# Performance work log

Measured on AMD Instinct MI355X. Metric: run time of the kernel, lower is better.

The kernel has to match this reference:

```python
import jax, jax.numpy as jnp
import numpy as np

B, K, D = 16384, 32, 64
N_USERS, N_ENT, N_REL = 100000, 100000, 32
MAX_NORM = 1.0


def renorm(e):
    # emulate torch nn.Embedding(max_norm=1): rescale rows with norm > 1
    n = jnp.linalg.norm(e, axis=-1, keepdims=True)
    return e * jnp.minimum(1.0, MAX_NORM / jnp.maximum(n, 1e-7))


def setup_inputs() -> dict:
    key = jax.random.key(0)
    ks = jax.random.split(key, 9)
    return {
        "user_table": jax.random.normal(ks[0], (N_USERS, D), dtype=jnp.float32),
        "entity_table": jax.random.normal(ks[1], (N_ENT, D), dtype=jnp.float32),
        "relation_table": jax.random.normal(ks[2], (N_REL, D), dtype=jnp.float32),
        "W": jax.random.normal(ks[3], (D, D), dtype=jnp.float32) / np.sqrt(D),
        "b": jnp.zeros((D,), dtype=jnp.float32),
        "users": jax.random.randint(ks[4], (B,), 0, N_USERS),
        "items": jax.random.randint(ks[5], (B,), 0, N_ENT),
        "adj_entity": jax.random.randint(ks[6], (N_ENT, K), 0, N_ENT),
        "adj_relation": jax.random.randint(ks[7], (N_ENT, K), 0, N_REL),
    }


def reference(user_table, entity_table, relation_table, W, b,
              users, items, adj_entity, adj_relation):
    # neighbor id gather: [B, K]
    nbr_ent_ids = adj_entity[items]
    nbr_rel_ids = adj_relation[items]
    # embedding lookups with max_norm renorm
    user_emb = renorm(user_table[users])                 # [B, D]
    item_emb = renorm(entity_table[items])               # [B, D]
    nbr_ent = renorm(entity_table[nbr_ent_ids])          # [B, K, D]
    nbr_rel = renorm(relation_table[nbr_rel_ids])        # [B, K, D]
    # user-relation attention scores, softmax over neighbors
    scores = jnp.einsum('bd,bkd->bk', user_emb, nbr_rel)  # [B, K]
    attn = jax.nn.softmax(scores, axis=-1)
    # attention-weighted neighbor aggregation
    nbr_vec = jnp.einsum('bk,bkd->bd', attn, nbr_ent)     # [B, D]
    # sum aggregator + linear + relu (dropout omitted: eval-mode baseline)
    out = item_emb + nbr_vec
    out = jax.nn.relu(out @ W.T + b)
    return (user_emb, out)
```

## Files before the change

kernel.cpp:

```cpp
#include <hip/hip_runtime.h>
#include <math.h>

#define BB 16384
#define KK_N 32
#define DD 64
#define N_ENT 100000
#define N_REL 32

#define WS_REL_OFF_BYTES ((size_t)N_ENT * DD * 2)
#define WS_NEED_BYTES (WS_REL_OFF_BYTES + (size_t)N_REL * DD * 4)

#define PT_ENT  N_ENT
#define PT_USER (N_ENT + BB)
#define PT_ALL  (N_ENT + BB + N_REL)

typedef _Float16 f16x8 __attribute__((ext_vector_type(8)));
typedef _Float16 f16x4 __attribute__((ext_vector_type(4)));
typedef float    f32x4 __attribute__((ext_vector_type(4)));

__device__ __forceinline__ float dot4(float4 a, float4 b) {
    return a.x * b.x + a.y * b.y + a.z * b.z + a.w * b.w;
}
__device__ __forceinline__ float red16(float ss) {
    ss += __shfl_xor(ss, 1, 64);
    ss += __shfl_xor(ss, 2, 64);
    ss += __shfl_xor(ss, 4, 64);
    ss += __shfl_xor(ss, 8, 64);
    return ss;
}
__device__ __forceinline__ unsigned short f2bf(float x) {
    unsigned int u = __float_as_uint(x);
    u += 0x7fffu + ((u >> 16) & 1u);
    return (unsigned short)(u >> 16);
}
__device__ __forceinline__ float bf2f(unsigned short h) {
    return __uint_as_float(((unsigned int)h) << 16);
}
__device__ __forceinline__ float4 bf4(ushort4 h) {
    return make_float4(bf2f(h.x), bf2f(h.y), bf2f(h.z), bf2f(h.w));
}

__global__ __launch_bounds__(256) void precompute(
    const float* __restrict__ user_table,
    const float* __restrict__ entity_table,
    const float* __restrict__ relation_table,
    const int*   __restrict__ users,
    unsigned short* __restrict__ ent_bf,
    float* __restrict__ rel_ws,
    float* __restrict__ out_user)
{
    const int tid = threadIdx.x;
    const int gl  = tid & 15;
    const int t   = blockIdx.x * 16 + (tid >> 4);
    if (t >= PT_ALL) return;

    if (t < PT_ENT) {
        float4 v = *reinterpret_cast<const float4*>(&entity_table[(size_t)t * DD + gl * 4]);
        float ss = red16(dot4(v, v));
        float sc = fminf(1.0f, __builtin_amdgcn_rsqf(ss));
        ushort4 h;
        h.x = f2bf(v.x * sc); h.y = f2bf(v.y * sc);
        h.z = f2bf(v.z * sc); h.w = f2bf(v.w * sc);
        *reinterpret_cast<ushort4*>(&ent_bf[(size_t)t * DD + gl * 4]) = h;
    } else if (t < PT_USER) {
        int u = t - PT_ENT;
        int uid = users[u];
        float4 v = *reinterpret_cast<const float4*>(&user_table[(size_t)uid * DD + gl * 4]);
        float ss = red16(dot4(v, v));
        float sc = fminf(1.0f, __builtin_amdgcn_rsqf(ss));
        v.x *= sc; v.y *= sc; v.z *= sc; v.w *= sc;
        *reinterpret_cast<float4*>(&out_user[(size_t)u * DD + gl * 4]) = v;
    } else {
        int rr = t - PT_USER;
        float4 v = *reinterpret_cast<const float4*>(&relation_table[rr * DD + gl * 4]);
        float ss = red16(dot4(v, v));
        float sc = fminf(1.0f, __builtin_amdgcn_rsqf(ss));
        v.x *= sc; v.y *= sc; v.z *= sc; v.w *= sc;
        *reinterpret_cast<float4*>(&rel_ws[rr * DD + ((gl * 4) ^ ((rr & 15) << 2))]) = v;
    }
}

__global__ __launch_bounds__(256) void kgcn_main(
    const unsigned short* __restrict__ ent_bf,
    const float* __restrict__ rel_ws,
    const float* __restrict__ W,
    const float* __restrict__ bias,
    const int*   __restrict__ items,
    const int*   __restrict__ adj_entity,
    const int*   __restrict__ adj_relation,
    const float* __restrict__ user_out,
    float* __restrict__ out_final)
{
    __shared__ __align__(16) float RelLds[N_REL * DD];
    __shared__ __align__(16) float Uv[4][4][64];
    __shared__ __align__(16) _Float16 Th[16][72];

    const int tid  = threadIdx.x;
    const int lane = tid & 63;
    const int wave = tid >> 6;
    const int grp  = lane >> 4;
    const int gl   = lane & 15;
    const int kk   = lane & 31;

    const int b0 = blockIdx.x * 16 + wave * 4;

    int iid[4];
    #pragma unroll
    for (int e = 0; e < 4; ++e)
        iid[e] = __builtin_amdgcn_readfirstlane(items[b0 + e]);

    const int* abase = (lane < 32) ? adj_entity : adj_relation;
    int adjv[4];
    #pragma unroll
    for (int e = 0; e < 4; ++e)
        adjv[e] = abase[(size_t)iid[e] * KK_N + kk];

    float4 uv[4];
    #pragma unroll
    for (int e = 0; e < 4; ++e)
        uv[e] = *reinterpret_cast<const float4*>(&user_out[(size_t)(b0 + e) * DD + gl * 4]);
    ushort4 itm[4];
    #pragma unroll
    for (int e = 0; e < 4; ++e)
        itm[e] = *reinterpret_cast<const ushort4*>(&ent_bf[(size_t)iid[e] * DD + gl * 4]);

    #pragma unroll
    for (int it = 0; it < 2; ++it)
        reinterpret_cast<float4*>(RelLds)[tid + it * 256] =
            reinterpret_cast<const float4*>(rel_ws)[tid + it * 256];
    __syncthreads();

    if (lane < 16) {
        #pragma unroll
        for (int e = 0; e < 4; ++e)
            *reinterpret_cast<float4*>(&Uv[wave][e][gl * 4]) = uv[e];
    }

    const int dbase = (lane >> 5) * 32;
    float wk[4];
    #pragma unroll
    for (int e = 0; e < 4; ++e) {
        const int rid  = __shfl(adjv[e], 32 + kk, 64);
        const int srel = (rid & 15) << 2;
        const float* relrow = &RelLds[rid * DD];
        float sc = 0.0f;
        #pragma unroll
        for (int d0 = 0; d0 < 32; d0 += 4) {
            int d = dbase + d0;
            float4 rv = *reinterpret_cast<const float4*>(&relrow[d ^ srel]);
            float4 tv = *reinterpret_cast<const float4*>(&Uv[wave][e][d]);
            sc += dot4(tv, rv);
        }
        sc += __shfl_xor(sc, 32, 64);
        float ex = __expf(sc);
        float sum = ex;
        #pragma unroll
        for (int m = 1; m < 32; m <<= 1) sum += __shfl_xor(sum, m, 64);
        wk[e] = ex * __builtin_amdgcn_rcpf(sum);
    }

    float4 acc[4];
    #pragma unroll
    for (int e = 0; e < 4; ++e) acc[e] = make_float4(0.f, 0.f, 0.f, 0.f);
    #pragma unroll
    for (int k0 = 0; k0 < 8; ++k0) {
        #pragma unroll
        for (int e = 0; e < 4; ++e) {
            int eid = adj_entity[(size_t)iid[e] * KK_N + k0 * 4 + grp];
            ushort4 r = *reinterpret_cast<const ushort4*>(&ent_bf[(size_t)eid * DD + gl * 4]);
            float c = __shfl(wk[e], k0 * 4 + grp, 64);
            float4 f = bf4(r);
            acc[e].x = fmaf(c, f.x, acc[e].x);
            acc[e].y = fmaf(c, f.y, acc[e].y);
            acc[e].z = fmaf(c, f.z, acc[e].z);
            acc[e].w = fmaf(c, f.w, acc[e].w);
        }
    }
    #pragma unroll
    for (int m = 16; m < 64; m <<= 1) {
        #pragma unroll
        for (int e = 0; e < 4; ++e) {
            acc[e].x += __shfl_xor(acc[e].x, m, 64);
            acc[e].y += __shfl_xor(acc[e].y, m, 64);
            acc[e].z += __shfl_xor(acc[e].z, m, 64);
            acc[e].w += __shfl_xor(acc[e].w, m, 64);
        }
    }

    if (lane < 16) {
        #pragma unroll
        for (int e = 0; e < 4; ++e) {
            float4 f = bf4(itm[e]);
            f16x4 h;
            h[0] = (_Float16)(f.x + acc[e].x);
            h[1] = (_Float16)(f.y + acc[e].y);
            h[2] = (_Float16)(f.z + acc[e].z);
            h[3] = (_Float16)(f.w + acc[e].w);
            *reinterpret_cast<f16x4*>(&Th[wave * 4 + e][gl * 4]) = h;
        }
    }
    __syncthreads();

    const int n0  = wave * 16;
    const int row = lane & 15;
    const int kg  = (lane >> 4) * 8;
    f32x4 d = {0.f, 0.f, 0.f, 0.f};
    #pragma unroll
    for (int kb = 0; kb < 64; kb += 32) {
        f16x8 a = *reinterpret_cast<const f16x8*>(&Th[row][kb + kg]);
        const float* wr = &W[(size_t)(n0 + row) * DD + kb + kg];
        float4 w0 = *reinterpret_cast<const float4*>(wr);
        float4 w1 = *reinterpret_cast<const float4*>(wr + 4);
        f16x8 bfr;
        bfr[0] = (_Float16)w0.x; bfr[1] = (_Float16)w0.y;
        bfr[2] = (_Float16)w0.z; bfr[3] = (_Float16)w0.w;
        bfr[4] = (_Float16)w1.x; bfr[5] = (_Float16)w1.y;
        bfr[6] = (_Float16)w1.z; bfr[7] = (_Float16)w1.w;
        d = __builtin_amdgcn_mfma_f32_16x16x32_f16(a, bfr, d, 0, 0, 0);
    }
    const float bcol = bias[n0 + row];
    #pragma unroll
    for (int r = 0; r < 4; ++r) {
        int orow = (lane >> 4) * 4 + r;
        int gb = blockIdx.x * 16 + orow;
        out_final[(size_t)gb * DD + n0 + row] = fmaxf(d[r] + bcol, 0.0f);
    }
}

__global__ __launch_bounds__(256) void kgcn_fused(
    const float* __restrict__ user_table,
    const float* __restrict__ entity_table,
    const float* __restrict__ relation_table,
    const float* __restrict__ W,
    const float* __restrict__ bias,
    const int*   __restrict__ users,
    const int*   __restrict__ items,
    const int*   __restrict__ adj_entity,
    const int*   __restrict__ adj_relation,
    float* __restrict__ out_user,
    float* __restrict__ out_final)
{
    __shared__ __align__(16) float Wlds[64 * 64];
    __shared__ __align__(16) float RelLds[N_REL * DD];
    __shared__ __align__(16) float Vec[4][64];

    const int tid  = threadIdx.x;
    const int lane = tid & 63;
    const int wave = tid >> 6;
    const int grp  = lane >> 4;
    const int gl   = lane & 15;

    const int b = blockIdx.x * 4 + wave;
    const int uid = __builtin_amdgcn_readfirstlane(users[b]);
    const int iid = __builtin_amdgcn_readfirstlane(items[b]);

    const int kk = lane & 31;
    const int* abase = (lane < 32) ? adj_entity : adj_relation;
    const int adjv = abase[(size_t)iid * KK_N + kk];
    float4 uv = *reinterpret_cast<const float4*>(&user_table[(size_t)uid * DD + gl * 4]);
    float4 iv = *reinterpret_cast<const float4*>(&entity_table[(size_t)iid * DD + gl * 4]);

    #pragma unroll
    for (int it = 0; it < 4; ++it) {
        int i = tid + it * 256;
        float4 w4 = reinterpret_cast<const float4*>(W)[i];
        int d = i >> 4;
        int j = (i & 15) * 4;
        *reinterpret_cast<float4*>(&Wlds[d * 64 + (j ^ ((d & 15) << 2))]) = w4;
    }
    #pragma unroll
    for (int it = 0; it < 2; ++it) {
        int r = wave * 8 + it * 4 + grp;
        float4 vv = reinterpret_cast<const float4*>(relation_table)[r * 16 + gl];
        float ss = red16(dot4(vv, vv));
        float sc = fminf(1.0f, __builtin_amdgcn_rsqf(ss));
        vv.x *= sc; vv.y *= sc; vv.z *= sc; vv.w *= sc;
        *reinterpret_cast<float4*>(&RelLds[r * 64 + ((gl * 4) ^ ((r & 15) << 2))]) = vv;
    }

    float ssu = red16(dot4(uv, uv));
    float usc = fminf(1.0f, __builtin_amdgcn_rsqf(ssu));
    uv.x *= usc; uv.y *= usc; uv.z *= usc; uv.w *= usc;
    if (lane < 16)
        *reinterpret_cast<float4*>(&out_user[(size_t)b * DD + gl * 4]) = uv;

    int eid[8];
    #pragma unroll
    for (int k0 = 0; k0 < 8; ++k0)
        eid[k0] = __shfl(adjv, k0 * 4 + grp, 64);
    float4 v[8];
    #pragma unroll
    for (int k0 = 0; k0 < 8; ++k0)
        v[k0] = *reinterpret_cast<const float4*>(&entity_table[(size_t)eid[k0] * DD + gl * 4]);

    __syncthreads();
    if (lane < 16)
        *reinterpret_cast<float4*>(&Vec[wave][gl * 4]) = uv;

    const int rid = __shfl(adjv, 32 + kk, 64);
    const int srel = (rid & 15) << 2;
    const float* relrow = &RelLds[rid * 64];
    const int dbase = (lane >> 5) * 32;
    float score = 0.0f;
    #pragma unroll
    for (int d0 = 0; d0 < 32; d0 += 4) {
        int d = dbase + d0;
        float4 rv = *reinterpret_cast<const float4*>(&relrow[d ^ srel]);
        float4 tv = *reinterpret_cast<const float4*>(&Vec[wave][d]);
        score += dot4(tv, rv);
    }
    score += __shfl_xor(score, 32, 64);

    float mx = score;
    #pragma unroll
    for (int m = 1; m < 32; m <<= 1) mx = fmaxf(mx, __shfl_xor(mx, m, 64));
    float e = __expf(score - mx);
    float sum = e;
    #pragma unroll
    for (int m = 1; m < 32; m <<= 1) sum += __shfl_xor(sum, m, 64);
    const float attn = e * __builtin_amdgcn_rcpf(sum);

    float cc[8];
    #pragma unroll
    for (int k0 = 0; k0 < 8; ++k0)
        cc[k0] = __shfl(attn, k0 * 4 + grp, 64);

    float4 acc = make_float4(0.f, 0.f, 0.f, 0.f);
    #pragma unroll
    for (int k0 = 0; k0 < 8; ++k0) {
        float ss = red16(dot4(v[k0], v[k0]));
        float sc = fminf(1.0f, __builtin_amdgcn_rsqf(ss));
        float ck = cc[k0] * sc;
        acc.x = fmaf(ck, v[k0].x, acc.x);
        acc.y = fmaf(ck, v[k0].y, acc.y);
        acc.z = fmaf(ck, v[k0].z, acc.z);
        acc.w = fmaf(ck, v[k0].w, acc.w);
    }
    #pragma unroll
    for (int m = 16; m < 64; m <<= 1) {
        acc.x += __shfl_xor(acc.x, m, 64);
        acc.y += __shfl_xor(acc.y, m, 64);
        acc.z += __shfl_xor(acc.z, m, 64);
        acc.w += __shfl_xor(acc.w, m, 64);
    }

    float ssi = red16(dot4(iv, iv));
    float isc = fminf(1.0f, __builtin_amdgcn_rsqf(ssi));
    float4 tmp;
    tmp.x = fmaf(isc, iv.x, acc.x);
    tmp.y = fmaf(isc, iv.y, acc.y);
    tmp.z = fmaf(isc, iv.z, acc.z);
    tmp.w = fmaf(isc, iv.w, acc.w);
    if (lane < 16)
        *reinterpret_cast<float4*>(&Vec[wave][gl * 4]) = tmp;

    const float bv = bias[lane];
    const float* wrow = &Wlds[lane * 64];
    const int twz = (lane & 15) << 2;
    float o = bv;
    #pragma unroll
    for (int j0 = 0; j0 < 64; j0 += 4) {
        float4 wv = *reinterpret_cast<const float4*>(&wrow[j0 ^ twz]);
        float4 tv = *reinterpret_cast<const float4*>(&Vec[wave][j0]);
        o += dot4(tv, wv);
    }
    out_final[(size_t)b * DD + lane] = fmaxf(o, 0.0f);
}

extern "C" void kernel_launch(void* const* d_in, const int* in_sizes, int n_in,
                              void* d_out, int out_size, void* d_ws, size_t ws_size,
                              hipStream_t stream)
{
    const float* user_table     = (const float*)d_in[0];
    const float* entity_table   = (const float*)d_in[1];
    const float* relation_table = (const float*)d_in[2];
    const float* W              = (const float*)d_in[3];
    const float* bias           = (const float*)d_in[4];
    const int*   users          = (const int*)d_in[5];
    const int*   items          = (const int*)d_in[6];
    const int*   adj_entity     = (const int*)d_in[7];
    const int*   adj_relation   = (const int*)d_in[8];

    float* out_user  = (float*)d_out;
    float* out_final = (float*)d_out + (size_t)BB * DD;

    if (ws_size >= WS_NEED_BYTES) {
        unsigned short* ent_bf = (unsigned short*)d_ws;
        float* rel_ws = (float*)((char*)d_ws + WS_REL_OFF_BYTES);
        precompute<<<(PT_ALL + 15) / 16, 256, 0, stream>>>(
            user_table, entity_table, relation_table, users, ent_bf, rel_ws, out_user);
        kgcn_main<<<BB / 16, 256, 0, stream>>>(
            ent_bf, rel_ws, W, bias, items, adj_entity, adj_relation, out_user, out_final);
    } else {
        kgcn_fused<<<BB / 4, 256, 0, stream>>>(user_table, entity_table, relation_table,
                                               W, bias, users, items, adj_entity, adj_relation,
                                               out_user, out_final);
    }
}
```

Before: 31.62 us.

## Assign one batch row per wave and prefetch neighbor rows before barrier

```diff
diff --git a/kernel.cpp b/kernel.cpp
--- a/kernel.cpp
+++ b/kernel.cpp
@@ -92,7 +92,7 @@
     float* __restrict__ out_final)
 {
     __shared__ __align__(16) float RelLds[N_REL * DD];
-    __shared__ __align__(16) float Uv[4][4][64];
+    __shared__ __align__(16) float Uv[4][64];
     __shared__ __align__(16) _Float16 Th[16][72];
 
     const int tid  = threadIdx.x;
@@ -102,27 +102,22 @@
     const int gl   = lane & 15;
     const int kk   = lane & 31;
 
-    const int b0 = blockIdx.x * 16 + wave * 4;
-
-    int iid[4];
-    #pragma unroll
-    for (int e = 0; e < 4; ++e)
-        iid[e] = __builtin_amdgcn_readfirstlane(items[b0 + e]);
+    const int b = blockIdx.x * 4 + wave;
+    const int iid = __builtin_amdgcn_readfirstlane(items[b]);
 
     const int* abase = (lane < 32) ? adj_entity : adj_relation;
-    int adjv[4];
-    #pragma unroll
-    for (int e = 0; e < 4; ++e)
-        adjv[e] = abase[(size_t)iid[e] * KK_N + kk];
-
-    float4 uv[4];
-    #pragma unroll
-    for (int e = 0; e < 4; ++e)
-        uv[e] = *reinterpret_cast<const float4*>(&user_out[(size_t)(b0 + e) * DD + gl * 4]);
-    ushort4 itm[4];
-    #pragma unroll
-    for (int e = 0; e < 4; ++e)
-        itm[e] = *reinterpret_cast<const ushort4*>(&ent_bf[(size_t)iid[e] * DD + gl * 4]);
+    const int adjv = abase[(size_t)iid * KK_N + kk];
+
+    int eid[8];
+    #pragma unroll
+    for (int k0 = 0; k0 < 8; ++k0)
+        eid[k0] = adj_entity[(size_t)iid * KK_N + k0 * 4 + grp];
+    ushort4 v[8];
+    #pragma unroll
+    for (int k0 = 0; k0 < 8; ++k0)
+        v[k0] = *reinterpret_cast<const ushort4*>(&ent_bf[(size_t)eid[k0] * DD + gl * 4]);
+    float4 uv = *reinterpret_cast<const float4*>(&user_out[(size_t)b * DD + gl * 4]);
+    ushort4 itm = *reinterpret_cast<const ushort4*>(&ent_bf[(size_t)iid * DD + gl * 4]);
 
     #pragma unroll
     for (int it = 0; it < 2; ++it)
@@ -130,74 +125,54 @@
             reinterpret_cast<const float4*>(rel_ws)[tid + it * 256];
     __syncthreads();
 
+    if (lane < 16)
+        *reinterpret_cast<float4*>(&Uv[wave][gl * 4]) = uv;
+
+    const int rid  = __shfl(adjv, 32 + kk, 64);
+    const int srel = (rid & 15) << 2;
+    const int dbase = (lane >> 5) * 32;
+    float s = 0.0f;
+    #pragma unroll
+    for (int d0 = 0; d0 < 32; d0 += 4) {
+        int d = dbase + d0;
+        float4 q = *reinterpret_cast<const float4*>(&Uv[wave][d]);
+        float4 r = *reinterpret_cast<const float4*>(&RelLds[rid * DD + (d ^ srel)]);
+        s += dot4(q, r);
+    }
+    s += __shfl_xor(s, 32, 64);
+
+    float e = __expf(s);
+    float sum = e;
+    #pragma unroll
+    for (int m = 1; m < 32; m <<= 1) sum += __shfl_xor(sum, m, 64);
+    const float wk = e * __builtin_amdgcn_rcpf(sum);
+
+    float4 acc = make_float4(0.f, 0.f, 0.f, 0.f);
+    #pragma unroll
+    for (int k0 = 0; k0 < 8; ++k0) {
+        float c = __shfl(wk, k0 * 4 + grp, 64);
+        float4 f = bf4(v[k0]);
+        acc.x = fmaf(c, f.x, acc.x);
+        acc.y = fmaf(c, f.y, acc.y);
+        acc.z = fmaf(c, f.z, acc.z);
+        acc.w = fmaf(c, f.w, acc.w);
+    }
+    #pragma unroll
+    for (int m = 16; m < 64; m <<= 1) {
+        acc.x += __shfl_xor(acc.x, m, 64);
+        acc.y += __shfl_xor(acc.y, m, 64);
+        acc.z += __shfl_xor(acc.z, m, 64);
+        acc.w += __shfl_xor(acc.w, m, 64);
+    }
+
     if (lane < 16) {
-        #pragma unroll
-        for (int e = 0; e < 4; ++e)
-            *reinterpret_cast<float4*>(&Uv[wave][e][gl * 4]) = uv[e];
-    }
-
-    const int dbase = (lane >> 5) * 32;
-    float wk[4];
-    #pragma unroll
-    for (int e = 0; e < 4; ++e) {
-        const int rid  = __shfl(adjv[e], 32 + kk, 64);
-        const int srel = (rid & 15) << 2;
-        const float* relrow = &RelLds[rid * DD];
-        float sc = 0.0f;
-        #pragma unroll
-        for (int d0 = 0; d0 < 32; d0 += 4) {
-            int d = dbase + d0;
-            float4 rv = *reinterpret_cast<const float4*>(&relrow[d ^ srel]);
-            float4 tv = *reinterpret_cast<const float4*>(&Uv[wave][e][d]);
-            sc += dot4(tv, rv);
-        }
-        sc += __shfl_xor(sc, 32, 64);
-        float ex = __expf(sc);
-        float sum = ex;
-        #pragma unroll
-        for (int m = 1; m < 32; m <<= 1) sum += __shfl_xor(sum, m, 64);
-        wk[e] = ex * __builtin_amdgcn_rcpf(sum);
-    }
-
-    float4 acc[4];
-    #pragma unroll
-    for (int e = 0; e < 4; ++e) acc[e] = make_float4(0.f, 0.f, 0.f, 0.f);
-    #pragma unroll
-    for (int k0 = 0; k0 < 8; ++k0) {
-        #pragma unroll
-        for (int e = 0; e < 4; ++e) {
-            int eid = adj_entity[(size_t)iid[e] * KK_N + k0 * 4 + grp];
-            ushort4 r = *reinterpret_cast<const ushort4*>(&ent_bf[(size_t)eid * DD + gl * 4]);
-            float c = __shfl(wk[e], k0 * 4 + grp, 64);
-            float4 f = bf4(r);
-            acc[e].x = fmaf(c, f.x, acc[e].x);
-            acc[e].y = fmaf(c, f.y, acc[e].y);
-            acc[e].z = fmaf(c, f.z, acc[e].z);
-            acc[e].w = fmaf(c, f.w, acc[e].w);
-        }
-    }
-    #pragma unroll
-    for (int m = 16; m < 64; m <<= 1) {
-        #pragma unroll
-        for (int e = 0; e < 4; ++e) {
-            acc[e].x += __shfl_xor(acc[e].x, m, 64);
-            acc[e].y += __shfl_xor(acc[e].y, m, 64);
-            acc[e].z += __shfl_xor(acc[e].z, m, 64);
-            acc[e].w += __shfl_xor(acc[e].w, m, 64);
-        }
-    }
-
-    if (lane < 16) {
-        #pragma unroll
-        for (int e = 0; e < 4; ++e) {
-            float4 f = bf4(itm[e]);
-            f16x4 h;
-            h[0] = (_Float16)(f.x + acc[e].x);
-            h[1] = (_Float16)(f.y + acc[e].y);
-            h[2] = (_Float16)(f.z + acc[e].z);
-            h[3] = (_Float16)(f.w + acc[e].w);
-            *reinterpret_cast<f16x4*>(&Th[wave * 4 + e][gl * 4]) = h;
-        }
+        float4 f = bf4(itm);
+        f16x4 h;
+        h[0] = (_Float16)(f.x + acc.x);
+        h[1] = (_Float16)(f.y + acc.y);
+        h[2] = (_Float16)(f.z + acc.z);
+        h[3] = (_Float16)(f.w + acc.w);
+        *reinterpret_cast<f16x4*>(&Th[wave][gl * 4]) = h;
     }
     __syncthreads();
 
@@ -219,11 +194,12 @@
         d = __builtin_amdgcn_mfma_f32_16x16x32_f16(a, bfr, d, 0, 0, 0);
     }
     const float bcol = bias[n0 + row];
-    #pragma unroll
-    for (int r = 0; r < 4; ++r) {
-        int orow = (lane >> 4) * 4 + r;
-        int gb = blockIdx.x * 16 + orow;
-        out_final[(size_t)gb * DD + n0 + row] = fmaxf(d[r] + bcol, 0.0f);
+    if (lane < 16) {
+        #pragma unroll
+        for (int r = 0; r < 4; ++r) {
+            int gb = blockIdx.x * 4 + r;
+            out_final[(size_t)gb * DD + n0 + row] = fmaxf(d[r] + bcol, 0.0f);
+        }
     }
 }
 
@@ -389,7 +365,7 @@
         float* rel_ws = (float*)((char*)d_ws + WS_REL_OFF_BYTES);
         precompute<<<(PT_ALL + 15) / 16, 256, 0, stream>>>(
             user_table, entity_table, relation_table, users, ent_bf, rel_ws, out_user);
-        kgcn_main<<<BB / 16, 256, 0, stream>>>(
+        kgcn_main<<<BB / 4, 256, 0, stream>>>(
             ent_bf, rel_ws, W, bias, items, adj_entity, adj_relation, out_user, out_final);
     } else {
         kgcn_fused<<<BB / 4, 256, 0, stream>>>(user_table, entity_table, relation_table,
```

New measurement: 32.55 us. 2.9% more time.
